# Kernel tuning notes

Hardware: AMD Instinct MI355X
Metric: run time of the kernel (lower is better)

## Reference

```python
import jax, jax.numpy as jnp
import numpy as np

S, B, H2 = 2048, 16, 1024   # seq_len, batch, 2*hidden_dim
H = H2 // 2                  # hidden_dim
N = 4096                     # number of spans with nonempty tags
T = 8192                     # total number of target tags (ragged, flattened)
L = 256                      # label_dim
V = 50000                    # vocab size
GAMMA = 1.0


def setup_inputs() -> dict:
    key = jax.random.key(0)
    ks = jax.random.split(key, 10)
    hidden = jax.random.normal(ks[0], (S, B, H2), jnp.float32)
    W1 = jax.random.normal(ks[1], (L, H2), jnp.float32) * (1.0 / np.sqrt(H2))
    b1 = jnp.zeros((L,), jnp.float32)
    W2 = jax.random.normal(ks[2], (V, L), jnp.float32) * (1.0 / np.sqrt(L))
    b2 = jnp.zeros((V,), jnp.float32)
    span_bid = jax.random.randint(ks[3], (N,), 0, B, jnp.int32)
    span_begin = jax.random.randint(ks[4], (N,), 0, S, jnp.int32)
    span_end = jax.random.randint(ks[5], (N,), 0, S, jnp.int32)
    tag_span_id = jax.random.randint(ks[6], (T,), 0, N, jnp.int32)
    tags = jax.random.randint(ks[7], (T,), 0, V, jnp.int32)
    return {"hidden": hidden, "W1": W1, "b1": b1, "W2": W2, "b2": b2,
            "span_bid": span_bid, "span_begin": span_begin,
            "span_end": span_end, "tag_span_id": tag_span_id, "tags": tags}


def reference(hidden, W1, b1, W2, b2, span_bid, span_begin, span_end,
              tag_span_id, tags):
    # span embedding: forward half at begin-1 (wraps like torch negative idx),
    # backward half at end.  -> [N, 2H]
    fwd = hidden[(span_begin - 1) % S, span_bid, :H]
    bwd = hidden[span_end, span_bid, H:]
    feat = jnp.concatenate([fwd, bwd], axis=-1)          # [N, 2H]
    x = jnp.tanh(feat @ W1.T + b1)                       # [N, L]  (Linear+Tanh)
    logits = x @ W2.T + b2                               # [N, V]
    logp = jax.nn.log_softmax(logits, axis=-1)           # stable softmax->log
    pos_logp = logp[tag_span_id, tags]                   # [T] gathered targets
    pos = jnp.exp(pos_logp)                              # positive_probs
    # focal loss, gamma=1: -(1-p)^gamma * log(p), summed over all tags
    loss = jnp.sum(-((1.0 - pos) ** GAMMA) * pos_logp)
    loss = loss / (jnp.float32(T) + 1e-5)
    return loss.reshape(1)
```

## Files before the change

### kernel.cpp

```cpp
#include <hip/hip_runtime.h>
#include <hip/hip_fp8.h>

#define S_    2048
#define B_    16
#define H2_   1024
#define H_    512
#define N_    4096
#define T_    8192
#define L_    256
#define V_    50000
#define VPAD_ 50048

#define LOG2E_ 1.44269504088896f

typedef float  floatx4 __attribute__((ext_vector_type(4)));
typedef __bf16 bf16x8  __attribute__((ext_vector_type(8)));
typedef int    intx4   __attribute__((ext_vector_type(4)));
typedef int    intx8   __attribute__((ext_vector_type(8)));

__device__ inline unsigned short f2bf(float f) {
  unsigned u = __builtin_bit_cast(unsigned, f);
  unsigned r = u + 0x7fffu + ((u >> 16) & 1u);
  return (unsigned short)(r >> 16);
}
__device__ inline float bf2f(unsigned short s) {
  unsigned u = ((unsigned)s) << 16;
  return __builtin_bit_cast(float, u);
}
__device__ inline unsigned char f2fp8(float f) {
  return (unsigned char)__hip_cvt_float_to_fp8(f, __HIP_SATFINITE, __HIP_E4M3);
}

__device__ inline void stage16(const void* g, void* l) {
  __builtin_amdgcn_global_load_lds(
      (const __attribute__((address_space(1))) void*)g,
      (__attribute__((address_space(3))) void*)l, 16, 0, 0);
}

__global__ __launch_bounds__(256) void gather_k(
    const float* __restrict__ hidden, const int* __restrict__ sbid,
    const int* __restrict__ sbeg, const int* __restrict__ send,
    unsigned short* __restrict__ featbf, float* __restrict__ lse) {
  const int n = blockIdx.x;
  const int t = threadIdx.x;
  if (t == 0) lse[n] = 0.f;
  if (n == 0 && t == 1) lse[N_] = 0.f;
  if (n == 0 && t == 2) ((unsigned*)lse)[N_ + 1] = 0u;
  const int bid = sbid[n];
  int r = sbeg[n] - 1; if (r < 0) r += S_;
  const int e = send[n];
  const size_t fbase = (size_t)r * (B_ * H2_) + (size_t)bid * H2_;
  const size_t bbase = (size_t)e * (B_ * H2_) + (size_t)bid * H2_;
  const int c = t * 4;
  const float4 v = (t < 128) ? *reinterpret_cast<const float4*>(hidden + fbase + c)
                             : *reinterpret_cast<const float4*>(hidden + bbase + c);
  unsigned short o[4];
  o[0] = f2bf(v.x); o[1] = f2bf(v.y); o[2] = f2bf(v.z); o[3] = f2bf(v.w);
  *reinterpret_cast<unsigned long long*>(featbf + (size_t)n * H2_ + c) =
      *reinterpret_cast<unsigned long long*>(o);
}

__global__ __launch_bounds__(256) void convert_k(
    const float* __restrict__ W1, const float* __restrict__ W2,
    const float* __restrict__ b2, unsigned short* __restrict__ w1b,
    unsigned char* __restrict__ w2f8, float* __restrict__ ebp) {
  const int gid = blockIdx.x * 256 + threadIdx.x;
  const int gstride = gridDim.x * 256;
  for (long j = (long)gid * 8; j < (long)VPAD_ * 256; j += (long)gstride * 8) {
    int row = (int)(j >> 8);
    unsigned char o[8];
    if (row < V_) {
#pragma unroll
      for (int q = 0; q < 8; q++) o[q] = f2fp8(W2[j + q] * LOG2E_);
    } else {
#pragma unroll
      for (int q = 0; q < 8; q++) o[q] = 0;
    }
    *reinterpret_cast<unsigned long long*>(w2f8 + j) =
        *reinterpret_cast<unsigned long long*>(o);
  }
  for (int j = gid; j < L_ * H2_; j += gstride) w1b[j] = f2bf(W1[j]);
  for (int j = gid; j < VPAD_; j += gstride) ebp[j] = (j < V_) ? __expf(b2[j]) : 0.f;
}

__global__ __launch_bounds__(256) void gemm1_k(
    const unsigned short* __restrict__ A,
    const unsigned short* __restrict__ Bw,
    const float* __restrict__ b1,
    unsigned short* __restrict__ xbf,
    unsigned char* __restrict__ xf8) {
  __shared__ __align__(16) unsigned short sA[64 * 64];
  __shared__ __align__(16) unsigned short sB[64 * 64];
  const int tid   = threadIdx.x;
  const int mtile = (int)(blockIdx.x >> 2) * 64;
  const int ntile = (int)(blockIdx.x & 3) * 64;
  const int lane = tid & 63, wave = tid >> 6;
  const int wr = (wave & 1) * 32, wc = (wave >> 1) * 32;
  const int fr = lane & 15, fq = lane >> 4;
  floatx4 acc[2][2] = {};
  for (int k0 = 0; k0 < H2_; k0 += 64) {
#pragma unroll
    for (int i = 0; i < 2; i++) {
      const int slot = tid + i * 256;
      const int r = slot >> 3, cc = slot & 7;
      const int gk = cc ^ (r & 7);
      stage16(A  + (size_t)(mtile + r) * H2_ + k0 + gk * 8, &sA[slot * 8]);
      stage16(Bw + (size_t)(ntile + r) * H2_ + k0 + gk * 8, &sB[slot * 8]);
    }
    __syncthreads();
#pragma unroll
    for (int ks = 0; ks < 2; ks++) {
      bf16x8 av[2], bv[2];
#pragma unroll
      for (int mi = 0; mi < 2; mi++) {
        const int r = wr + mi * 16 + fr, kc = ks * 4 + fq;
        av[mi] = *reinterpret_cast<const bf16x8*>(&sA[(r * 8 + (kc ^ (r & 7))) * 8]);
      }
#pragma unroll
      for (int ni = 0; ni < 2; ni++) {
        const int r = wc + ni * 16 + fr, kc = ks * 4 + fq;
        bv[ni] = *reinterpret_cast<const bf16x8*>(&sB[(r * 8 + (kc ^ (r & 7))) * 8]);
      }
#pragma unroll
      for (int mi = 0; mi < 2; mi++)
#pragma unroll
        for (int ni = 0; ni < 2; ni++)
          acc[mi][ni] = __builtin_amdgcn_mfma_f32_16x16x32_bf16(av[mi], bv[ni], acc[mi][ni], 0, 0, 0);
    }
    __syncthreads();
  }
#pragma unroll
  for (int ni = 0; ni < 2; ni++) {
    const int col = ntile + wc + ni * 16 + fr;
    const float bias = b1[col];
#pragma unroll
    for (int mi = 0; mi < 2; mi++)
#pragma unroll
      for (int r = 0; r < 4; r++) {
        const int row = mtile + wr + mi * 16 + fq * 4 + r;
        const float t = tanhf(acc[mi][ni][r] + bias);
        xbf[(size_t)row * L_ + col] = f2bf(t);
        xf8[(size_t)row * L_ + col] = f2fp8(t);
      }
  }
}

__global__ __launch_bounds__(512, 4) void gemm2_k(
    const unsigned char* __restrict__ X8,
    const unsigned char* __restrict__ W8,
    const float* __restrict__ ebp,
    float* __restrict__ lse_sum) {
  __shared__ __align__(16) unsigned char sB[2][32768];
  const int tid   = threadIdx.x;
  const int mtile = ((int)blockIdx.x >> 4) * 128;
  const int strip = (int)blockIdx.x & 15;
  const int vt0   = (strip < 7) ? strip * 25 : 175 + (strip - 7) * 24;
  const int nt    = (strip < 7) ? 25 : 24;
  const int lane = tid & 63, wave = tid >> 6;
  const int wr = (wave & 3) * 32;
  const int wc = (wave >> 2) * 64;
  const int fr = lane & 15, fq = lane >> 4;

#pragma unroll
  for (int i = 0; i < 4; i++) {
    const int slot = tid + i * 512;
    const int r = slot >> 4, c = slot & 15;
    stage16(X8 + (size_t)(mtile + r) * 256 + ((c ^ (r & 15)) << 4), &sB[0][slot << 4]);
  }
  __syncthreads();
  intx8 af[2][2];
#pragma unroll
  for (int mi = 0; mi < 2; mi++)
#pragma unroll
    for (int kh = 0; kh < 2; kh++) {
      const int r  = wr + mi * 16 + fr;
      const int c0 = kh * 8 + fq * 2;
      *reinterpret_cast<intx4*>(&af[mi][kh]) =
          *reinterpret_cast<const intx4*>(&sB[0][(r << 8) + ((c0 ^ (r & 15)) << 4)]);
      *(reinterpret_cast<intx4*>(&af[mi][kh]) + 1) =
          *reinterpret_cast<const intx4*>(&sB[0][(r << 8) + (((c0 + 1) ^ (r & 15)) << 4)]);
    }
  __syncthreads();

  float sacc[2][4];
#pragma unroll
  for (int mi = 0; mi < 2; mi++)
#pragma unroll
    for (int r = 0; r < 4; r++) sacc[mi][r] = 0.f;

  float eb_cur[4], eb_nxt[4];
#pragma unroll
  for (int ni = 0; ni < 4; ni++)
    eb_nxt[ni] = ebp[vt0 * 128 + wc + ni * 16 + fr];
  {
    const unsigned char* base = W8 + (size_t)vt0 * 128 * 256;
#pragma unroll
    for (int i = 0; i < 4; i++) {
      const int slot = tid + i * 512;
      const int r = slot >> 4, c = slot & 15;
      stage16(base + ((size_t)r << 8) + ((c ^ (r & 15)) << 4), &sB[0][slot << 4]);
    }
  }

  for (int j = 0; j < nt; j++) {
#pragma unroll
    for (int ni = 0; ni < 4; ni++) eb_cur[ni] = eb_nxt[ni];
    __syncthreads();
    if (j + 1 < nt) {
      const int vt = vt0 + j + 1;
#pragma unroll
      for (int ni = 0; ni < 4; ni++)
        eb_nxt[ni] = ebp[vt * 128 + wc + ni * 16 + fr];
      const unsigned char* base = W8 + (size_t)vt * 128 * 256;
      unsigned char* dst = &sB[(j + 1) & 1][0];
#pragma unroll
      for (int i = 0; i < 4; i++) {
        const int slot = tid + i * 512;
        const int r = slot >> 4, c = slot & 15;
        stage16(base + ((size_t)r << 8) + ((c ^ (r & 15)) << 4), dst + (slot << 4));
      }
    }

    const unsigned char* bb = &sB[j & 1][0];
    floatx4 acc[2][4] = {};
#pragma unroll
    for (int kh = 0; kh < 2; kh++) {
#pragma unroll
      for (int ni = 0; ni < 4; ni++) {
        intx8 bv;
        const int r  = wc + ni * 16 + fr;
        const int c0 = kh * 8 + fq * 2;
        *reinterpret_cast<intx4*>(&bv) =
            *reinterpret_cast<const intx4*>(&bb[(r << 8) + ((c0 ^ (r & 15)) << 4)]);
        *(reinterpret_cast<intx4*>(&bv) + 1) =
            *reinterpret_cast<const intx4*>(&bb[(r << 8) + (((c0 + 1) ^ (r & 15)) << 4)]);
#pragma unroll
        for (int mi = 0; mi < 2; mi++)
          acc[mi][ni] = __builtin_amdgcn_mfma_scale_f32_16x16x128_f8f6f4(
              af[mi][kh], bv, acc[mi][ni], 0, 0,
              0, 0x7f7f7f7f, 0, 0x7f7f7f7f);
      }
    }
#pragma unroll
    for (int mi = 0; mi < 2; mi++)
#pragma unroll
      for (int r = 0; r < 4; r++) {
        float s = sacc[mi][r];
#pragma unroll
        for (int ni = 0; ni < 4; ni++)
          s = fmaf(eb_cur[ni], __builtin_amdgcn_exp2f(acc[mi][ni][r]), s);
        sacc[mi][r] = s;
      }
  }

#pragma unroll
  for (int mi = 0; mi < 2; mi++)
#pragma unroll
    for (int r = 0; r < 4; r++) {
      float s = sacc[mi][r];
      s += __shfl_xor(s, 1);
      s += __shfl_xor(s, 2);
      s += __shfl_xor(s, 4);
      s += __shfl_xor(s, 8);
      if (fr == 0)
        atomicAdd(&lse_sum[mtile + wr + mi * 16 + fq * 4 + r], s);
    }
}

__global__ __launch_bounds__(256) void loss_k(
    const unsigned short* __restrict__ xbf, const float* __restrict__ W2,
    const float* __restrict__ b2, const int* __restrict__ tsid,
    const int* __restrict__ tags, const float* __restrict__ lse_sum,
    float* __restrict__ loss_acc, unsigned* __restrict__ ticket,
    float* __restrict__ out) {
  const int lane = threadIdx.x & 63;
  const int gw = (int)(blockIdx.x * 256 + threadIdx.x) >> 6;
  const int nw = (int)(gridDim.x * 256) >> 6;
  float total = 0.f;
  for (int t = gw; t < T_; t += nw) {
    const int sid = tsid[t];
    const int v   = tags[t];
    const unsigned short* xr = xbf + (size_t)sid * L_;
    const float* w2r = W2 + (size_t)v * L_;
    float d = 0.f;
#pragma unroll
    for (int q = 0; q < 4; q++) {
      const int j = lane * 4 + q;
      d += bf2f(xr[j]) * w2r[j];
    }
#pragma unroll
    for (int m = 1; m < 64; m <<= 1) d += __shfl_xor(d, m);
    const float lp  = d + b2[v] - logf(lse_sum[sid]);
    const float pos = __expf(lp);
    total += (pos - 1.f) * lp;
  }
  if (lane == 0) atomicAdd(loss_acc, total);
  __syncthreads();
  __threadfence();
  if (threadIdx.x == 0) {
    const unsigned t = atomicAdd(ticket, 1u);
    if (t == (unsigned)gridDim.x - 1u) {
      const float v = atomicAdd(loss_acc, 0.0f);
      out[0] = v / (8192.0f + 1e-5f);
    }
  }
}

extern "C" void kernel_launch(void* const* d_in, const int* in_sizes, int n_in,
                              void* d_out, int out_size, void* d_ws, size_t ws_size,
                              hipStream_t stream) {
  const float* hidden = (const float*)d_in[0];
  const float* W1     = (const float*)d_in[1];
  const float* b1     = (const float*)d_in[2];
  const float* W2     = (const float*)d_in[3];
  const float* b2     = (const float*)d_in[4];
  const int* sbid = (const int*)d_in[5];
  const int* sbeg = (const int*)d_in[6];
  const int* send = (const int*)d_in[7];
  const int* tsid = (const int*)d_in[8];
  const int* tags = (const int*)d_in[9];
  float* out = (float*)d_out;

  char* ws = (char*)d_ws;
  unsigned short* featbf = (unsigned short*)(ws);
  unsigned short* xbf    = (unsigned short*)(ws + 8388608);
  unsigned short* w1bf   = (unsigned short*)(ws + 10485760);
  unsigned char*  xf8    = (unsigned char*) (ws + 11010048);
  unsigned char*  w2f8   = (unsigned char*) (ws + 12058624);
  float* ebp  = (float*)(ws + 24870912);
  float* lse  = (float*)(ws + 25071104);
  float* lacc = lse + N_;
  unsigned* ticket = (unsigned*)(lse + N_ + 1);

  gather_k<<<dim3(N_), dim3(256), 0, stream>>>(hidden, sbid, sbeg, send, featbf, lse);
  convert_k<<<dim3(4096), dim3(256), 0, stream>>>(W1, W2, b2, w1bf, w2f8, ebp);
  gemm1_k<<<dim3(256), dim3(256), 0, stream>>>(featbf, w1bf, b1, xbf, xf8);
  gemm2_k<<<dim3(512), dim3(512), 0, stream>>>(xf8, w2f8, ebp, lse);
  loss_k<<<dim3(256), dim3(256), 0, stream>>>(xbf, W2, b2, tsid, tags, lse, lacc, ticket, out);
}
```

Measured before the change: 310.4 us.

## Fuse gather/convert kernels, shrink GEMM tiles for more blocks, vectorize loss loads

```diff
diff --git a/kernel.cpp b/kernel.cpp
--- a/kernel.cpp
+++ b/kernel.cpp
@@ -37,35 +37,36 @@
       (__attribute__((address_space(3))) void*)l, 16, 0, 0);
 }
 
-__global__ __launch_bounds__(256) void gather_k(
+__global__ __launch_bounds__(256) void prep_k(
     const float* __restrict__ hidden, const int* __restrict__ sbid,
     const int* __restrict__ sbeg, const int* __restrict__ send,
-    unsigned short* __restrict__ featbf, float* __restrict__ lse) {
-  const int n = blockIdx.x;
-  const int t = threadIdx.x;
-  if (t == 0) lse[n] = 0.f;
-  if (n == 0 && t == 1) lse[N_] = 0.f;
-  if (n == 0 && t == 2) ((unsigned*)lse)[N_ + 1] = 0u;
-  const int bid = sbid[n];
-  int r = sbeg[n] - 1; if (r < 0) r += S_;
-  const int e = send[n];
-  const size_t fbase = (size_t)r * (B_ * H2_) + (size_t)bid * H2_;
-  const size_t bbase = (size_t)e * (B_ * H2_) + (size_t)bid * H2_;
-  const int c = t * 4;
-  const float4 v = (t < 128) ? *reinterpret_cast<const float4*>(hidden + fbase + c)
-                             : *reinterpret_cast<const float4*>(hidden + bbase + c);
-  unsigned short o[4];
-  o[0] = f2bf(v.x); o[1] = f2bf(v.y); o[2] = f2bf(v.z); o[3] = f2bf(v.w);
-  *reinterpret_cast<unsigned long long*>(featbf + (size_t)n * H2_ + c) =
-      *reinterpret_cast<unsigned long long*>(o);
-}
-
-__global__ __launch_bounds__(256) void convert_k(
+    unsigned short* __restrict__ featbf, float* __restrict__ lse,
     const float* __restrict__ W1, const float* __restrict__ W2,
     const float* __restrict__ b2, unsigned short* __restrict__ w1b,
     unsigned char* __restrict__ w2f8, float* __restrict__ ebp) {
-  const int gid = blockIdx.x * 256 + threadIdx.x;
-  const int gstride = gridDim.x * 256;
+  const int blk = (int)blockIdx.x;
+  const int t = threadIdx.x;
+  if (blk < N_) {
+    const int n = blk;
+    if (t == 0) lse[n] = 0.f;
+    if (n == 0 && t == 1) lse[N_] = 0.f;
+    if (n == 0 && t == 2) ((unsigned*)lse)[N_ + 1] = 0u;
+    const int bid = sbid[n];
+    int r = sbeg[n] - 1; if (r < 0) r += S_;
+    const int e = send[n];
+    const size_t fbase = (size_t)r * (B_ * H2_) + (size_t)bid * H2_;
+    const size_t bbase = (size_t)e * (B_ * H2_) + (size_t)bid * H2_;
+    const int c = t * 4;
+    const float4 v = (t < 128) ? *reinterpret_cast<const float4*>(hidden + fbase + c)
+                               : *reinterpret_cast<const float4*>(hidden + bbase + c);
+    unsigned short o[4];
+    o[0] = f2bf(v.x); o[1] = f2bf(v.y); o[2] = f2bf(v.z); o[3] = f2bf(v.w);
+    *reinterpret_cast<unsigned long long*>(featbf + (size_t)n * H2_ + c) =
+        *reinterpret_cast<unsigned long long*>(o);
+    return;
+  }
+  const int gid = (blk - N_) * 256 + t;
+  const int gstride = 4096 * 256;
   for (long j = (long)gid * 8; j < (long)VPAD_ * 256; j += (long)gstride * 8) {
     int row = (int)(j >> 8);
     unsigned char o[8];
@@ -89,32 +90,36 @@
     const float* __restrict__ b1,
     unsigned short* __restrict__ xbf,
     unsigned char* __restrict__ xf8) {
-  __shared__ __align__(16) unsigned short sA[64 * 64];
+  __shared__ __align__(16) unsigned short sA[32 * 64];
   __shared__ __align__(16) unsigned short sB[64 * 64];
   const int tid   = threadIdx.x;
-  const int mtile = (int)(blockIdx.x >> 2) * 64;
+  const int mtile = (int)(blockIdx.x >> 2) * 32;
   const int ntile = (int)(blockIdx.x & 3) * 64;
   const int lane = tid & 63, wave = tid >> 6;
-  const int wr = (wave & 1) * 32, wc = (wave >> 1) * 32;
+  const int wr = (wave & 1) * 16;
+  const int wc = (wave >> 1) * 32;
   const int fr = lane & 15, fq = lane >> 4;
-  floatx4 acc[2][2] = {};
+  floatx4 acc[2] = {};
   for (int k0 = 0; k0 < H2_; k0 += 64) {
+    {
+      const int r = tid >> 3, cc = tid & 7;
+      const int gk = cc ^ (r & 7);
+      stage16(A + (size_t)(mtile + r) * H2_ + k0 + gk * 8, &sA[tid * 8]);
+    }
 #pragma unroll
     for (int i = 0; i < 2; i++) {
       const int slot = tid + i * 256;
       const int r = slot >> 3, cc = slot & 7;
       const int gk = cc ^ (r & 7);
-      stage16(A  + (size_t)(mtile + r) * H2_ + k0 + gk * 8, &sA[slot * 8]);
       stage16(Bw + (size_t)(ntile + r) * H2_ + k0 + gk * 8, &sB[slot * 8]);
     }
     __syncthreads();
 #pragma unroll
     for (int ks = 0; ks < 2; ks++) {
-      bf16x8 av[2], bv[2];
-#pragma unroll
-      for (int mi = 0; mi < 2; mi++) {
-        const int r = wr + mi * 16 + fr, kc = ks * 4 + fq;
-        av[mi] = *reinterpret_cast<const bf16x8*>(&sA[(r * 8 + (kc ^ (r & 7))) * 8]);
+      bf16x8 av, bv[2];
+      {
+        const int r = wr + fr, kc = ks * 4 + fq;
+        av = *reinterpret_cast<const bf16x8*>(&sA[(r * 8 + (kc ^ (r & 7))) * 8]);
       }
 #pragma unroll
       for (int ni = 0; ni < 2; ni++) {
@@ -122,10 +127,8 @@
         bv[ni] = *reinterpret_cast<const bf16x8*>(&sB[(r * 8 + (kc ^ (r & 7))) * 8]);
       }
 #pragma unroll
-      for (int mi = 0; mi < 2; mi++)
-#pragma unroll
-        for (int ni = 0; ni < 2; ni++)
-          acc[mi][ni] = __builtin_amdgcn_mfma_f32_16x16x32_bf16(av[mi], bv[ni], acc[mi][ni], 0, 0, 0);
+      for (int ni = 0; ni < 2; ni++)
+        acc[ni] = __builtin_amdgcn_mfma_f32_16x16x32_bf16(av, bv[ni], acc[ni], 0, 0, 0);
     }
     __syncthreads();
   }
@@ -134,38 +137,37 @@
     const int col = ntile + wc + ni * 16 + fr;
     const float bias = b1[col];
 #pragma unroll
-    for (int mi = 0; mi < 2; mi++)
-#pragma unroll
-      for (int r = 0; r < 4; r++) {
-        const int row = mtile + wr + mi * 16 + fq * 4 + r;
-        const float t = tanhf(acc[mi][ni][r] + bias);
-        xbf[(size_t)row * L_ + col] = f2bf(t);
-        xf8[(size_t)row * L_ + col] = f2fp8(t);
-      }
-  }
-}
-
-__global__ __launch_bounds__(512, 4) void gemm2_k(
+    for (int r = 0; r < 4; r++) {
+      const int row = mtile + wr + fq * 4 + r;
+      const float t = tanhf(acc[ni][r] + bias);
+      xbf[(size_t)row * L_ + col] = f2bf(t);
+      xf8[(size_t)row * L_ + col] = f2fp8(t);
+    }
+  }
+}
+
+__global__ __launch_bounds__(512, 6) void gemm2_k(
     const unsigned char* __restrict__ X8,
     const unsigned char* __restrict__ W8,
     const float* __restrict__ ebp,
     float* __restrict__ lse_sum) {
-  __shared__ __align__(16) unsigned char sB[2][32768];
+  __shared__ __align__(16) unsigned char sB[2][16384];
+  unsigned char* sAll = &sB[0][0];
   const int tid   = threadIdx.x;
-  const int mtile = ((int)blockIdx.x >> 4) * 128;
-  const int strip = (int)blockIdx.x & 15;
-  const int vt0   = (strip < 7) ? strip * 25 : 175 + (strip - 7) * 24;
-  const int nt    = (strip < 7) ? 25 : 24;
+  const int mtile = ((int)blockIdx.x >> 5) * 128;
+  const int strip = (int)blockIdx.x & 31;
+  const int vt0   = (strip < 14) ? strip * 25 : 350 + (strip - 14) * 24;
+  const int nt    = (strip < 14) ? 25 : 24;
   const int lane = tid & 63, wave = tid >> 6;
   const int wr = (wave & 3) * 32;
-  const int wc = (wave >> 2) * 64;
+  const int wc = (wave >> 2) * 32;
   const int fr = lane & 15, fq = lane >> 4;
 
 #pragma unroll
   for (int i = 0; i < 4; i++) {
     const int slot = tid + i * 512;
     const int r = slot >> 4, c = slot & 15;
-    stage16(X8 + (size_t)(mtile + r) * 256 + ((c ^ (r & 15)) << 4), &sB[0][slot << 4]);
+    stage16(X8 + (size_t)(mtile + r) * 256 + ((c ^ (r & 15)) << 4), &sAll[slot << 4]);
   }
   __syncthreads();
   intx8 af[2][2];
@@ -176,9 +178,9 @@
       const int r  = wr + mi * 16 + fr;
       const int c0 = kh * 8 + fq * 2;
       *reinterpret_cast<intx4*>(&af[mi][kh]) =
-          *reinterpret_cast<const intx4*>(&sB[0][(r << 8) + ((c0 ^ (r & 15)) << 4)]);
+          *reinterpret_cast<const intx4*>(&sAll[(r << 8) + ((c0 ^ (r & 15)) << 4)]);
       *(reinterpret_cast<intx4*>(&af[mi][kh]) + 1) =
-          *reinterpret_cast<const intx4*>(&sB[0][(r << 8) + (((c0 + 1) ^ (r & 15)) << 4)]);
+          *reinterpret_cast<const intx4*>(&sAll[(r << 8) + (((c0 + 1) ^ (r & 15)) << 4)]);
     }
   __syncthreads();
 
@@ -188,14 +190,14 @@
 #pragma unroll
     for (int r = 0; r < 4; r++) sacc[mi][r] = 0.f;
 
-  float eb_cur[4], eb_nxt[4];
-#pragma unroll
-  for (int ni = 0; ni < 4; ni++)
-    eb_nxt[ni] = ebp[vt0 * 128 + wc + ni * 16 + fr];
+  float eb_cur[2], eb_nxt[2];
+#pragma unroll
+  for (int ni = 0; ni < 2; ni++)
+    eb_nxt[ni] = ebp[vt0 * 64 + wc + ni * 16 + fr];
   {
-    const unsigned char* base = W8 + (size_t)vt0 * 128 * 256;
-#pragma unroll
-    for (int i = 0; i < 4; i++) {
+    const unsigned char* base = W8 + ((size_t)vt0 << 14);
+#pragma unroll
+    for (int i = 0; i < 2; i++) {
       const int slot = tid + i * 512;
       const int r = slot >> 4, c = slot & 15;
       stage16(base + ((size_t)r << 8) + ((c ^ (r & 15)) << 4), &sB[0][slot << 4]);
@@ -204,17 +206,17 @@
 
   for (int j = 0; j < nt; j++) {
 #pragma unroll
-    for (int ni = 0; ni < 4; ni++) eb_cur[ni] = eb_nxt[ni];
+    for (int ni = 0; ni < 2; ni++) eb_cur[ni] = eb_nxt[ni];
     __syncthreads();
     if (j + 1 < nt) {
       const int vt = vt0 + j + 1;
 #pragma unroll
-      for (int ni = 0; ni < 4; ni++)
-        eb_nxt[ni] = ebp[vt * 128 + wc + ni * 16 + fr];
-      const unsigned char* base = W8 + (size_t)vt * 128 * 256;
+      for (int ni = 0; ni < 2; ni++)
+        eb_nxt[ni] = ebp[vt * 64 + wc + ni * 16 + fr];
+      const unsigned char* base = W8 + ((size_t)vt << 14);
       unsigned char* dst = &sB[(j + 1) & 1][0];
 #pragma unroll
-      for (int i = 0; i < 4; i++) {
+      for (int i = 0; i < 2; i++) {
         const int slot = tid + i * 512;
         const int r = slot >> 4, c = slot & 15;
         stage16(base + ((size_t)r << 8) + ((c ^ (r & 15)) << 4), dst + (slot << 4));
@@ -222,11 +224,12 @@
     }
 
     const unsigned char* bb = &sB[j & 1][0];
-    floatx4 acc[2][4] = {};
+    floatx4 acc[2][2] = {};
+    __builtin_amdgcn_s_setprio(1);
 #pragma unroll
     for (int kh = 0; kh < 2; kh++) {
 #pragma unroll
-      for (int ni = 0; ni < 4; ni++) {
+      for (int ni = 0; ni < 2; ni++) {
         intx8 bv;
         const int r  = wc + ni * 16 + fr;
         const int c0 = kh * 8 + fq * 2;
@@ -241,13 +244,14 @@
               0, 0x7f7f7f7f, 0, 0x7f7f7f7f);
       }
     }
+    __builtin_amdgcn_s_setprio(0);
 #pragma unroll
     for (int mi = 0; mi < 2; mi++)
 #pragma unroll
       for (int r = 0; r < 4; r++) {
         float s = sacc[mi][r];
 #pragma unroll
-        for (int ni = 0; ni < 4; ni++)
+        for (int ni = 0; ni < 2; ni++)
           s = fmaf(eb_cur[ni], __builtin_amdgcn_exp2f(acc[mi][ni][r]), s);
         sacc[mi][r] = s;
       }
@@ -282,12 +286,13 @@
     const int v   = tags[t];
     const unsigned short* xr = xbf + (size_t)sid * L_;
     const float* w2r = W2 + (size_t)v * L_;
-    float d = 0.f;
-#pragma unroll
-    for (int q = 0; q < 4; q++) {
-      const int j = lane * 4 + q;
-      d += bf2f(xr[j]) * w2r[j];
-    }
+    const unsigned long long xv =
+        *reinterpret_cast<const unsigned long long*>(xr + (lane << 2));
+    const float4 wv = *reinterpret_cast<const float4*>(w2r + (lane << 2));
+    float d = bf2f((unsigned short)xv) * wv.x
+            + bf2f((unsigned short)(xv >> 16)) * wv.y
+            + bf2f((unsigned short)(xv >> 32)) * wv.z
+            + bf2f((unsigned short)(xv >> 48)) * wv.w;
 #pragma unroll
     for (int m = 1; m < 64; m <<= 1) d += __shfl_xor(d, m);
     const float lp  = d + b2[v] - logf(lse_sum[sid]);
@@ -332,9 +337,9 @@
   float* lacc = lse + N_;
   unsigned* ticket = (unsigned*)(lse + N_ + 1);
 
-  gather_k<<<dim3(N_), dim3(256), 0, stream>>>(hidden, sbid, sbeg, send, featbf, lse);
-  convert_k<<<dim3(4096), dim3(256), 0, stream>>>(W1, W2, b2, w1bf, w2f8, ebp);
-  gemm1_k<<<dim3(256), dim3(256), 0, stream>>>(featbf, w1bf, b1, xbf, xf8);
-  gemm2_k<<<dim3(512), dim3(512), 0, stream>>>(xf8, w2f8, ebp, lse);
-  loss_k<<<dim3(256), dim3(256), 0, stream>>>(xbf, W2, b2, tsid, tags, lse, lacc, ticket, out);
-}
+  prep_k<<<dim3(8192), dim3(256), 0, stream>>>(hidden, sbid, sbeg, send, featbf, lse,
+                                               W1, W2, b2, w1bf, w2f8, ebp);
+  gemm1_k<<<dim3(512), dim3(256), 0, stream>>>(featbf, w1bf, b1, xbf, xf8);
+  gemm2_k<<<dim3(1024), dim3(512), 0, stream>>>(xf8, w2f8, ebp, lse);
+  loss_k<<<dim3(512), dim3(256), 0, stream>>>(xbf, W2, b2, tsid, tags, lse, lacc, ticket, out);
+}
```

Measured after the change: 432.1 us. +39.2%, slower.
